# Kernel tuning notes

Hardware: AMD Instinct MI355X
Metric: run time of the kernel (lower is better)

## Reference

```python
import jax, jax.numpy as jnp
import numpy as np

D = 768          # hidden_size
N_HEADS = 12
HEAD_DIM = D // N_HEADS  # 64
WINDOW = 128 // 2        # local_attention // 2 = 64 tokens each side
ROPE_THETA = 10000.0     # local_rope_theta


def _rope_freqs(T, dtype=jnp.float32):
    # complex rotation factors e^{i * pos * inv_freq}, shape [T, HEAD_DIM//2]
    inv_freq = 1.0 / (ROPE_THETA ** (jnp.arange(0, HEAD_DIM, 2, dtype=dtype) / HEAD_DIM))
    ang = jnp.arange(T, dtype=dtype)[:, None] * inv_freq[None, :]
    return jnp.exp(1j * ang.astype(jnp.complex64))


def _apply_rope(x, freqs):
    # x: [B, T, N, H]; split into (2, H//2) pairs as in the source reshape
    B, T, N, H = x.shape
    pairs = x.reshape(B, T, N, 2, H // 2)
    c = pairs[..., 0, :] + 1j * pairs[..., 1, :]          # [B,T,N,H//2]
    rot = c * freqs[None, :, None, :]                      # broadcast over B, heads
    out = jnp.stack([jnp.real(rot), jnp.imag(rot)], axis=-1)  # [B,T,N,H//2,2]
    return out.reshape(B, T, N, H)  # attention_scaling = 1.0 for default rope


def setup_inputs() -> dict:
    key = jax.random.key(0)
    k1, k2, k3 = jax.random.split(key, 3)
    B, T = 4, 2048
    hidden_states = jax.random.normal(k1, (B, T, D), dtype=jnp.float32)
    attention_mask = jnp.ones((B, T), dtype=jnp.int32)
    Wqkv = jax.random.normal(k2, (3 * D, D), dtype=jnp.float32) * (1.0 / np.sqrt(D))
    Wo = jax.random.normal(k3, (D, D), dtype=jnp.float32) * (1.0 / np.sqrt(D))
    return {"hidden_states": hidden_states, "attention_mask": attention_mask,
            "Wqkv": Wqkv, "Wo": Wo}


def reference(hidden_states, attention_mask, Wqkv, Wo):
    B, T, _ = hidden_states.shape
    # fused QKV projection (no bias in ModernBERT)
    qkv = jnp.einsum('btd,ed->bte', hidden_states, Wqkv)   # [B,T,3D]
    q, k, v = jnp.split(qkv, 3, axis=-1)
    to_heads = lambda x: x.reshape(B, T, N_HEADS, HEAD_DIM)
    q, k, v = to_heads(q), to_heads(k), to_heads(v)
    # rotary embedding (complex multiply)
    freqs = _rope_freqs(T)
    q = _apply_rope(q, freqs)
    k = _apply_rope(k, freqs)
    # sliding-window + padding mask
    pos = jnp.arange(T)
    window = jnp.abs(pos[:, None] - pos[None, :]) <= WINDOW   # [T,T]
    pad = attention_mask.astype(jnp.bool_)                    # [B,T]
    allowed = window[None, None, :, :] & pad[:, None, :, None] & pad[:, None, None, :]
    # eager SDPA
    scale = 1.0 / np.sqrt(HEAD_DIM)
    scores = jnp.einsum('bqnh,bknh->bnqk', q, k) * scale      # [B,N,T,T]
    scores = jnp.where(allowed, scores, jnp.finfo(scores.dtype).min)
    probs = jax.nn.softmax(scores, axis=-1)
    attn = jnp.einsum('bnqk,bknh->bqnh', probs, v)            # [B,T,N,H]
    attn = attn.reshape(B, T, D)
    return jnp.einsum('btd,ed->bte', attn, Wo)                # output proj
```

## Files before the change

### kernel.cpp

```cpp
#include <hip/hip_runtime.h>
#include <hip/hip_bf16.h>
#include <math.h>

#define BATCH 4
#define SEQ   2048
#define DMODEL 768
#define NHEADS 12
#define HDIM  64
#define WIN   64
#define QKV_LD 2304

typedef __attribute__((ext_vector_type(8))) short bf16x8;
typedef __attribute__((ext_vector_type(4))) float f32x4;

typedef __attribute__((address_space(1))) const unsigned int guint;
typedef __attribute__((address_space(3))) unsigned int luint;

__device__ inline void gl_lds16(const __hip_bfloat16* g, __hip_bfloat16* l) {
    __builtin_amdgcn_global_load_lds((guint*)g, (luint*)l, 16, 0, 0);
}

__device__ inline void store_out(float* p, float v) { *p = v; }
__device__ inline void store_out(__hip_bfloat16* p, float v) { *p = __float2bfloat16(v); }

#define N4_HID  (BATCH * SEQ * DMODEL / 4)
#define N4_WQKV (QKV_LD * DMODEL / 4)
#define N4_WO   (DMODEL * DMODEL / 4)
#define N_ROPE  (SEQ * 32)
#define SETUP_TOTAL (N4_HID + N4_WQKV + N4_WO + N_ROPE)

__device__ inline void cast4(const float* in, __hip_bfloat16* out, int i) {
    float4 v = ((const float4*)in)[i];
    union { ushort4 u; __hip_bfloat16 h[4]; } o;
    o.h[0] = __float2bfloat16(v.x); o.h[1] = __float2bfloat16(v.y);
    o.h[2] = __float2bfloat16(v.z); o.h[3] = __float2bfloat16(v.w);
    ((ushort4*)out)[i] = o.u;
}

__global__ __launch_bounds__(256) void setup_kernel(const float* __restrict__ hidden,
                                                    const float* __restrict__ Wqkv,
                                                    const float* __restrict__ Wo,
                                                    __hip_bfloat16* __restrict__ hid_bf,
                                                    __hip_bfloat16* __restrict__ wqkv_bf,
                                                    __hip_bfloat16* __restrict__ wo_bf,
                                                    float2* __restrict__ tab) {
    int id = blockIdx.x * 256 + threadIdx.x;
    if (id < N4_HID) {
        cast4(hidden, hid_bf, id);
    } else if (id < N4_HID + N4_WQKV) {
        cast4(Wqkv, wqkv_bf, id - N4_HID);
    } else if (id < N4_HID + N4_WQKV + N4_WO) {
        cast4(Wo, wo_bf, id - N4_HID - N4_WQKV);
    } else if (id < SETUP_TOTAL) {
        int idx = id - (N4_HID + N4_WQKV + N4_WO);
        int t = idx >> 5, j = idx & 31;
        const float L2T_OVER_32 = 13.287712379549449f / 32.0f;
        float inv = exp2f(-(float)j * L2T_OVER_32);
        float s, c;
        sincosf((float)t * inv, &s, &c);
        tab[idx] = make_float2(c, s);
    }
}

template <typename OutT>
__global__ __launch_bounds__(256) void gemm_nt_bf16(const __hip_bfloat16* __restrict__ A,
                                                    const __hip_bfloat16* __restrict__ B,
                                                    OutT* __restrict__ C,
                                                    int lda, int ldb, int ldc, int K,
                                                    const float2* __restrict__ rope_tab) {
    __shared__ __align__(16) __hip_bfloat16 As[128 * 32];
    __shared__ __align__(16) __hip_bfloat16 Bs[128 * 32];

    const int tid  = threadIdx.x;
    const int lane = tid & 63;
    const int wave = tid >> 6;
    const int wr   = wave >> 1;
    const int wc   = wave & 1;
    const int fr   = lane & 15;
    const int quad = lane >> 4;

    const int bid = blockIdx.x;
    const int x   = bid & 7;
    const int j   = bid >> 3;
    const int m0  = (x * 8 + (j & 7)) * 128;
    const int n0  = (j >> 3) * 128;

    f32x4 acc[4][4];
#pragma unroll
    for (int i = 0; i < 4; i++)
#pragma unroll
        for (int jj = 0; jj < 4; jj++) acc[i][jj] = (f32x4){0.f, 0.f, 0.f, 0.f};

    for (int k0 = 0; k0 < K; k0 += 32) {
        __syncthreads();
#pragma unroll
        for (int c = 0; c < 2; c++) {
            int e = (wave * 2 + c) * 512 + lane * 8;
            int row = e >> 5, col = e & 31;
            gl_lds16(A + (size_t)(m0 + row) * lda + k0 + col, As + e);
            gl_lds16(B + (size_t)(n0 + row) * ldb + k0 + col, Bs + e);
        }
        __syncthreads();

        bf16x8 af[4], bf_[4];
#pragma unroll
        for (int mi = 0; mi < 4; mi++)
            af[mi] = *(const bf16x8*)(As + (wr * 64 + mi * 16 + fr) * 32 + quad * 8);
#pragma unroll
        for (int ni = 0; ni < 4; ni++)
            bf_[ni] = *(const bf16x8*)(Bs + (wc * 64 + ni * 16 + fr) * 32 + quad * 8);
#pragma unroll
        for (int mi = 0; mi < 4; mi++)
#pragma unroll
            for (int ni = 0; ni < 4; ni++)
                acc[mi][ni] = __builtin_amdgcn_mfma_f32_16x16x32_bf16(af[mi], bf_[ni], acc[mi][ni], 0, 0, 0);
    }

    const int b0 = n0 + wc * 64;
    if (rope_tab != nullptr && b0 < 2 * DMODEL) {
#pragma unroll
        for (int mi = 0; mi < 4; mi++) {
#pragma unroll
            for (int r = 0; r < 4; r++) {
                int t = (m0 + wr * 64 + mi * 16 + quad * 4 + r) & (SEQ - 1);
#pragma unroll
                for (int ni = 0; ni < 2; ni++) {
                    float2 cs = rope_tab[t * 32 + ni * 16 + fr];
                    float x0 = acc[mi][ni][r], x1 = acc[mi][ni + 2][r];
                    acc[mi][ni][r]     = x0 * cs.x - x1 * cs.y;
                    acc[mi][ni + 2][r] = x0 * cs.y + x1 * cs.x;
                }
            }
        }
    }

#pragma unroll
    for (int mi = 0; mi < 4; mi++)
#pragma unroll
        for (int ni = 0; ni < 4; ni++) {
            f32x4 v = acc[mi][ni];
            int gc = b0 + ni * 16 + fr;
            size_t rbase = (size_t)(m0 + wr * 64 + mi * 16 + quad * 4);
#pragma unroll
            for (int r = 0; r < 4; r++)
                store_out(&C[(rbase + r) * ldc + gc], v[r]);
        }
}

#define KSLD 72
#define PLD  192

__global__ __launch_bounds__(256) void attn_kernel(const __hip_bfloat16* __restrict__ qkv,
                                                   const int* __restrict__ mask,
                                                   __hip_bfloat16* __restrict__ attn) {
    __shared__ __align__(16) char smem[61440];
    __hip_bfloat16* Ks = (__hip_bfloat16*)smem;
    __hip_bfloat16* Pb = (__hip_bfloat16*)smem;
    __hip_bfloat16* Qs = (__hip_bfloat16*)(smem + 27648);
    __hip_bfloat16* Vt = (__hip_bfloat16*)(smem + 36864);

    const int tid  = threadIdx.x;
    const int lane = tid & 63;
    const int wave = tid >> 6;
    const int fr   = lane & 15;
    const int quad = lane >> 4;

    const int bid  = blockIdx.x;
    const int x    = bid & 7;
    const int j    = bid >> 3;
    const int b    = x >> 1;
    const int q0   = ((x & 1) * 16 + (j & 15)) * 64;
    const int head = j >> 4;

    const int klo = max(0, q0 - WIN);
    const int khi = min(SEQ, q0 + 64 + WIN);
    const int nk  = khi - klo;
    const int nt  = nk >> 4;
    const int nkc = nk >> 5;

    const size_t rowbase = (size_t)(b * SEQ) * QKV_LD + head * HDIM;

#pragma unroll
    for (int it = 0; it < 2; it++) {
        int task = tid + it * 256;
        int row = task >> 3, g = task & 7;
        uint4 v = *(const uint4*)(qkv + rowbase + (size_t)(q0 + row) * QKV_LD + g * 8);
        *(uint4*)(Qs + row * KSLD + g * 8) = v;
    }
    for (int task = tid; task < nk * 8; task += 256) {
        int row = task >> 3, g = task & 7;
        uint4 v = *(const uint4*)(qkv + rowbase + (size_t)(klo + row) * QKV_LD + DMODEL + g * 8);
        *(uint4*)(Ks + row * KSLD + g * 8) = v;
    }
    {
        int h = lane;
        const __hip_bfloat16* vb = qkv + rowbase + 2 * DMODEL + h;
        int ng = nk >> 3;
        for (int g = wave; g < ng; g += 4) {
            unsigned int u0, u1, u2, u3;
            {
                unsigned short a0 = *(const unsigned short*)(vb + (size_t)(klo + g * 8 + 0) * QKV_LD);
                unsigned short a1 = *(const unsigned short*)(vb + (size_t)(klo + g * 8 + 1) * QKV_LD);
                unsigned short a2 = *(const unsigned short*)(vb + (size_t)(klo + g * 8 + 2) * QKV_LD);
                unsigned short a3 = *(const unsigned short*)(vb + (size_t)(klo + g * 8 + 3) * QKV_LD);
                unsigned short a4 = *(const unsigned short*)(vb + (size_t)(klo + g * 8 + 4) * QKV_LD);
                unsigned short a5 = *(const unsigned short*)(vb + (size_t)(klo + g * 8 + 5) * QKV_LD);
                unsigned short a6 = *(const unsigned short*)(vb + (size_t)(klo + g * 8 + 6) * QKV_LD);
                unsigned short a7 = *(const unsigned short*)(vb + (size_t)(klo + g * 8 + 7) * QKV_LD);
                u0 = (unsigned int)a0 | ((unsigned int)a1 << 16);
                u1 = (unsigned int)a2 | ((unsigned int)a3 << 16);
                u2 = (unsigned int)a4 | ((unsigned int)a5 << 16);
                u3 = (unsigned int)a6 | ((unsigned int)a7 << 16);
            }
            int cs = g ^ (h & 7);
            *(uint4*)(Vt + h * PLD + cs * 8) = make_uint4(u0, u1, u2, u3);
        }
    }
    __syncthreads();

    const int qrow0 = q0 + wave * 16;
    bf16x8 aq0 = *(const bf16x8*)(Qs + (wave * 16 + fr) * KSLD + quad * 8);
    bf16x8 aq1 = *(const bf16x8*)(Qs + (wave * 16 + fr) * KSLD + 32 + quad * 8);

    const int* mb = mask + b * SEQ;
    int mq[4];
#pragma unroll
    for (int r = 0; r < 4; r++) mq[r] = mb[qrow0 + quad * 4 + r];

    f32x4 sc[12];
#pragma unroll
    for (int kt = 0; kt < 12; kt++) sc[kt] = (f32x4){-1e30f, -1e30f, -1e30f, -1e30f};

#pragma unroll
    for (int kt = 0; kt < 12; kt++) {
        if (kt < nt) {
            int kg = klo + kt * 16 + fr;
            bf16x8 b0 = *(const bf16x8*)(Ks + (kt * 16 + fr) * KSLD + quad * 8);
            bf16x8 b1 = *(const bf16x8*)(Ks + (kt * 16 + fr) * KSLD + 32 + quad * 8);
            f32x4 a = (f32x4){0.f, 0.f, 0.f, 0.f};
            a = __builtin_amdgcn_mfma_f32_16x16x32_bf16(aq0, b0, a, 0, 0, 0);
            a = __builtin_amdgcn_mfma_f32_16x16x32_bf16(aq1, b1, a, 0, 0, 0);
            int mk = mb[kg];
            f32x4 s;
#pragma unroll
            for (int r = 0; r < 4; r++) {
                int qg = qrow0 + quad * 4 + r;
                bool ok = (abs(qg - kg) <= WIN) && (mk != 0) && (mq[r] != 0);
                s[r] = ok ? a[r] * 0.125f : -1e30f;
            }
            sc[kt] = s;
        }
    }

    f32x4 mx = sc[0];
#pragma unroll
    for (int kt = 1; kt < 12; kt++)
#pragma unroll
        for (int r = 0; r < 4; r++) mx[r] = fmaxf(mx[r], sc[kt][r]);
#pragma unroll
    for (int off = 8; off >= 1; off >>= 1)
#pragma unroll
        for (int r = 0; r < 4; r++) mx[r] = fmaxf(mx[r], __shfl_xor(mx[r], off));

    f32x4 sum = (f32x4){0.f, 0.f, 0.f, 0.f};
#pragma unroll
    for (int kt = 0; kt < 12; kt++)
#pragma unroll
        for (int r = 0; r < 4; r++) {
            float e = __expf(sc[kt][r] - mx[r]);
            sc[kt][r] = e;
            sum[r] += e;
        }
#pragma unroll
    for (int off = 8; off >= 1; off >>= 1)
#pragma unroll
        for (int r = 0; r < 4; r++) sum[r] += __shfl_xor(sum[r], off);
    f32x4 rs;
#pragma unroll
    for (int r = 0; r < 4; r++) rs[r] = 1.0f / sum[r];

    __syncthreads();
#pragma unroll
    for (int kt = 0; kt < 12; kt++) {
        if (kt < nt) {
#pragma unroll
            for (int r = 0; r < 4; r++) {
                int prow = wave * 16 + quad * 4 + r;
                int c = kt * 2 + (fr >> 3);
                int cs = c ^ (prow & 7);
                Pb[prow * PLD + cs * 8 + (fr & 7)] = __float2bfloat16(sc[kt][r] * rs[r]);
            }
        }
    }
    __syncthreads();

    f32x4 o[4];
#pragma unroll
    for (int ht = 0; ht < 4; ht++) o[ht] = (f32x4){0.f, 0.f, 0.f, 0.f};

#pragma unroll
    for (int kc = 0; kc < 6; kc++) {
        if (kc < nkc) {
            int cs = (kc * 4 + quad) ^ (fr & 7);
            bf16x8 ap = *(const bf16x8*)(Pb + (wave * 16 + fr) * PLD + cs * 8);
#pragma unroll
            for (int ht = 0; ht < 4; ht++) {
                bf16x8 bv = *(const bf16x8*)(Vt + (ht * 16 + fr) * PLD + cs * 8);
                o[ht] = __builtin_amdgcn_mfma_f32_16x16x32_bf16(ap, bv, o[ht], 0, 0, 0);
            }
        }
    }

    __hip_bfloat16* ob = attn + (size_t)(b * SEQ + qrow0) * DMODEL + head * HDIM;
#pragma unroll
    for (int r = 0; r < 4; r++)
#pragma unroll
        for (int ht = 0; ht < 4; ht++)
            ob[(size_t)(quad * 4 + r) * DMODEL + ht * 16 + fr] = __float2bfloat16(o[ht][r]);
}

extern "C" void kernel_launch(void* const* d_in, const int* in_sizes, int n_in,
                              void* d_out, int out_size, void* d_ws, size_t ws_size,
                              hipStream_t stream) {
    const float* hidden = (const float*)d_in[0];
    const int*   mask   = (const int*)d_in[1];
    const float* Wqkv   = (const float*)d_in[2];
    const float* Wo     = (const float*)d_in[3];
    float* out = (float*)d_out;

    char* w = (char*)d_ws;
    __hip_bfloat16* qkv_bf  = (__hip_bfloat16*)(w);
    __hip_bfloat16* hid_bf  = (__hip_bfloat16*)(w + 37748736);
    __hip_bfloat16* wqkv_bf = (__hip_bfloat16*)(w + 50331648);
    __hip_bfloat16* wo_bf   = (__hip_bfloat16*)(w + 53870592);
    __hip_bfloat16* attn_bf = (__hip_bfloat16*)(w + 55050240);
    float2*         tab     = (float2*)(w + 67633152);

    setup_kernel<<<SETUP_TOTAL / 256, 256, 0, stream>>>(hidden, Wqkv, Wo,
                                                        hid_bf, wqkv_bf, wo_bf, tab);

    gemm_nt_bf16<__hip_bfloat16><<<18 * 64, 256, 0, stream>>>(hid_bf, wqkv_bf, qkv_bf,
                                                              DMODEL, DMODEL, QKV_LD, DMODEL, tab);

    attn_kernel<<<(SEQ / 64) * NHEADS * BATCH, 256, 0, stream>>>(qkv_bf, mask, attn_bf);

    gemm_nt_bf16<float><<<6 * 64, 256, 0, stream>>>(attn_bf, wo_bf, out,
                                                    DMODEL, DMODEL, DMODEL, DMODEL, nullptr);
}
```

Before: 194.0 us.

## Deepen GEMM K-tile with XOR-swizzled LDS, stage stores, load Q directly in attention

```diff
diff --git a/kernel.cpp b/kernel.cpp
--- a/kernel.cpp
+++ b/kernel.cpp
@@ -20,8 +20,8 @@
     __builtin_amdgcn_global_load_lds((guint*)g, (luint*)l, 16, 0, 0);
 }
 
-__device__ inline void store_out(float* p, float v) { *p = v; }
-__device__ inline void store_out(__hip_bfloat16* p, float v) { *p = __float2bfloat16(v); }
+__device__ inline void to_out(float* p, float v) { *p = v; }
+__device__ inline void to_out(__hip_bfloat16* p, float v) { *p = __float2bfloat16(v); }
 
 #define N4_HID  (BATCH * SEQ * DMODEL / 4)
 #define N4_WQKV (QKV_LD * DMODEL / 4)
@@ -68,8 +68,9 @@
                                                     OutT* __restrict__ C,
                                                     int lda, int ldb, int ldc, int K,
                                                     const float2* __restrict__ rope_tab) {
-    __shared__ __align__(16) __hip_bfloat16 As[128 * 32];
-    __shared__ __align__(16) __hip_bfloat16 Bs[128 * 32];
+    __shared__ __align__(16) char smem[32768];
+    __hip_bfloat16* As = (__hip_bfloat16*)smem;
+    __hip_bfloat16* Bs = (__hip_bfloat16*)(smem + 16384);
 
     const int tid  = threadIdx.x;
     const int lane = tid & 63;
@@ -91,29 +92,39 @@
 #pragma unroll
         for (int jj = 0; jj < 4; jj++) acc[i][jj] = (f32x4){0.f, 0.f, 0.f, 0.f};
 
-    for (int k0 = 0; k0 < K; k0 += 32) {
+    for (int k0 = 0; k0 < K; k0 += 64) {
         __syncthreads();
 #pragma unroll
-        for (int c = 0; c < 2; c++) {
-            int e = (wave * 2 + c) * 512 + lane * 8;
-            int row = e >> 5, col = e & 31;
-            gl_lds16(A + (size_t)(m0 + row) * lda + k0 + col, As + e);
-            gl_lds16(B + (size_t)(n0 + row) * ldb + k0 + col, Bs + e);
+        for (int c = 0; c < 4; c++) {
+            int t = (wave * 4 + c) * 64 + lane;
+            int row = t >> 3, ch = t & 7;
+            int gcol = (ch ^ (row & 7)) * 8;
+            gl_lds16(A + (size_t)(m0 + row) * lda + k0 + gcol, As + t * 8);
+            gl_lds16(B + (size_t)(n0 + row) * ldb + k0 + gcol, Bs + t * 8);
         }
         __syncthreads();
 
-        bf16x8 af[4], bf_[4];
-#pragma unroll
-        for (int mi = 0; mi < 4; mi++)
-            af[mi] = *(const bf16x8*)(As + (wr * 64 + mi * 16 + fr) * 32 + quad * 8);
-#pragma unroll
-        for (int ni = 0; ni < 4; ni++)
-            bf_[ni] = *(const bf16x8*)(Bs + (wc * 64 + ni * 16 + fr) * 32 + quad * 8);
-#pragma unroll
-        for (int mi = 0; mi < 4; mi++)
-#pragma unroll
-            for (int ni = 0; ni < 4; ni++)
-                acc[mi][ni] = __builtin_amdgcn_mfma_f32_16x16x32_bf16(af[mi], bf_[ni], acc[mi][ni], 0, 0, 0);
+#pragma unroll
+        for (int ks = 0; ks < 2; ks++) {
+            bf16x8 af[4], bf_[4];
+#pragma unroll
+            for (int mi = 0; mi < 4; mi++) {
+                int row = wr * 64 + mi * 16 + fr;
+                int pos = (ks * 4 + quad) ^ (row & 7);
+                af[mi] = *(const bf16x8*)(As + row * 64 + pos * 8);
+            }
+#pragma unroll
+            for (int ni = 0; ni < 4; ni++) {
+                int row = wc * 64 + ni * 16 + fr;
+                int pos = (ks * 4 + quad) ^ (row & 7);
+                bf_[ni] = *(const bf16x8*)(Bs + row * 64 + pos * 8);
+            }
+#pragma unroll
+            for (int mi = 0; mi < 4; mi++)
+#pragma unroll
+                for (int ni = 0; ni < 4; ni++)
+                    acc[mi][ni] = __builtin_amdgcn_mfma_f32_16x16x32_bf16(af[mi], bf_[ni], acc[mi][ni], 0, 0, 0);
+        }
     }
 
     const int b0 = n0 + wc * 64;
@@ -134,30 +145,39 @@
         }
     }
 
-#pragma unroll
-    for (int mi = 0; mi < 4; mi++)
-#pragma unroll
-        for (int ni = 0; ni < 4; ni++) {
-            f32x4 v = acc[mi][ni];
-            int gc = b0 + ni * 16 + fr;
-            size_t rbase = (size_t)(m0 + wr * 64 + mi * 16 + quad * 4);
+    __syncthreads();
+    OutT* patch = (OutT*)smem + wave * (16 * 72);
+    constexpr int NV = sizeof(OutT);
+
+#pragma unroll
+    for (int mi = 0; mi < 4; mi++) {
+#pragma unroll
+        for (int ni = 0; ni < 4; ni++)
 #pragma unroll
             for (int r = 0; r < 4; r++)
-                store_out(&C[(rbase + r) * ldc + gc], v[r]);
-        }
-}
-
-#define KSLD 72
+                to_out(&patch[(quad * 4 + r) * 72 + ni * 16 + fr], acc[mi][ni][r]);
+        __syncthreads();
+        {
+            int prow = lane >> 2, seg = lane & 3;
+            const uint4* src = (const uint4*)(patch + prow * 72 + seg * 16);
+            OutT* dst = &C[(size_t)(m0 + wr * 64 + mi * 16 + prow) * ldc + b0 + seg * 16];
+#pragma unroll
+            for (int v = 0; v < NV; v++)
+                ((uint4*)dst)[v] = src[v];
+        }
+        __syncthreads();
+    }
+}
+
 #define PLD  192
 
 __global__ __launch_bounds__(256) void attn_kernel(const __hip_bfloat16* __restrict__ qkv,
                                                    const int* __restrict__ mask,
                                                    __hip_bfloat16* __restrict__ attn) {
-    __shared__ __align__(16) char smem[61440];
+    __shared__ __align__(16) char smem[49152];
     __hip_bfloat16* Ks = (__hip_bfloat16*)smem;
     __hip_bfloat16* Pb = (__hip_bfloat16*)smem;
-    __hip_bfloat16* Qs = (__hip_bfloat16*)(smem + 27648);
-    __hip_bfloat16* Vt = (__hip_bfloat16*)(smem + 36864);
+    __hip_bfloat16* Vt = (__hip_bfloat16*)(smem + 24576);
 
     const int tid  = threadIdx.x;
     const int lane = tid & 63;
@@ -180,17 +200,10 @@
 
     const size_t rowbase = (size_t)(b * SEQ) * QKV_LD + head * HDIM;
 
-#pragma unroll
-    for (int it = 0; it < 2; it++) {
-        int task = tid + it * 256;
-        int row = task >> 3, g = task & 7;
-        uint4 v = *(const uint4*)(qkv + rowbase + (size_t)(q0 + row) * QKV_LD + g * 8);
-        *(uint4*)(Qs + row * KSLD + g * 8) = v;
-    }
     for (int task = tid; task < nk * 8; task += 256) {
         int row = task >> 3, g = task & 7;
         uint4 v = *(const uint4*)(qkv + rowbase + (size_t)(klo + row) * QKV_LD + DMODEL + g * 8);
-        *(uint4*)(Ks + row * KSLD + g * 8) = v;
+        *(uint4*)(Ks + row * 64 + (g ^ (row & 7)) * 8) = v;
     }
     {
         int h = lane;
@@ -216,17 +229,18 @@
             *(uint4*)(Vt + h * PLD + cs * 8) = make_uint4(u0, u1, u2, u3);
         }
     }
-    __syncthreads();
 
     const int qrow0 = q0 + wave * 16;
-    bf16x8 aq0 = *(const bf16x8*)(Qs + (wave * 16 + fr) * KSLD + quad * 8);
-    bf16x8 aq1 = *(const bf16x8*)(Qs + (wave * 16 + fr) * KSLD + 32 + quad * 8);
+    bf16x8 aq0 = *(const bf16x8*)(qkv + rowbase + (size_t)(qrow0 + fr) * QKV_LD + quad * 8);
+    bf16x8 aq1 = *(const bf16x8*)(qkv + rowbase + (size_t)(qrow0 + fr) * QKV_LD + 32 + quad * 8);
 
     const int* mb = mask + b * SEQ;
     int mq[4];
 #pragma unroll
     for (int r = 0; r < 4; r++) mq[r] = mb[qrow0 + quad * 4 + r];
 
+    __syncthreads();
+
     f32x4 sc[12];
 #pragma unroll
     for (int kt = 0; kt < 12; kt++) sc[kt] = (f32x4){-1e30f, -1e30f, -1e30f, -1e30f};
@@ -234,12 +248,15 @@
 #pragma unroll
     for (int kt = 0; kt < 12; kt++) {
         if (kt < nt) {
-            int kg = klo + kt * 16 + fr;
-            bf16x8 b0 = *(const bf16x8*)(Ks + (kt * 16 + fr) * KSLD + quad * 8);
-            bf16x8 b1 = *(const bf16x8*)(Ks + (kt * 16 + fr) * KSLD + 32 + quad * 8);
+            int krow = kt * 16 + fr;
+            int kg = klo + krow;
+            int p0 = (quad) ^ (krow & 7);
+            int p1 = (4 + quad) ^ (krow & 7);
+            bf16x8 bk0 = *(const bf16x8*)(Ks + krow * 64 + p0 * 8);
+            bf16x8 bk1 = *(const bf16x8*)(Ks + krow * 64 + p1 * 8);
             f32x4 a = (f32x4){0.f, 0.f, 0.f, 0.f};
-            a = __builtin_amdgcn_mfma_f32_16x16x32_bf16(aq0, b0, a, 0, 0, 0);
-            a = __builtin_amdgcn_mfma_f32_16x16x32_bf16(aq1, b1, a, 0, 0, 0);
+            a = __builtin_amdgcn_mfma_f32_16x16x32_bf16(aq0, bk0, a, 0, 0, 0);
+            a = __builtin_amdgcn_mfma_f32_16x16x32_bf16(aq1, bk1, a, 0, 0, 0);
             int mk = mb[kg];
             f32x4 s;
 #pragma unroll
```

New measurement: 192.1 us. No clear change (-1.0%).
